# Optimization experiments

Measured on AMD Instinct MI355X. Metric: run time of the kernel, lower is better.

The kernel has to match this reference:

```python
import jax, jax.numpy as jnp
import numpy as np

CAPACITY_FACTOR = 1.0


def setup_inputs() -> dict:
    key = jax.random.key(0)
    k1, k2, k3, k4 = jax.random.split(key, 4)
    B, T, D, E, F = 4, 2048, 2048, 8, 8192
    hidden_states = jax.random.normal(k1, (B, T, D), dtype=jnp.float32)
    w_gate = jax.random.normal(k2, (D, E), dtype=jnp.float32) * 0.02
    w1 = jax.random.normal(k3, (E, D, F), dtype=jnp.float32) * 0.02
    w2 = jax.random.normal(k4, (E, F, D), dtype=jnp.float32) * 0.02
    return {"hidden_states": hidden_states, "w_gate": w_gate, "w1": w1, "w2": w2}


def _top1_gate(x, w_gate):
    # x: [S, D]; deepspeed top1gating (no noise, no rts, drop_tokens=True)
    S, E = x.shape[0], w_gate.shape[1]
    capacity = int(CAPACITY_FACTOR * S / E)
    logits = x @ w_gate                      # [S, E]
    gates = jax.nn.softmax(logits, axis=-1)  # [S, E]
    idx1 = jnp.argmax(gates, axis=-1)        # [S]
    mask1 = jax.nn.one_hot(idx1, E, dtype=gates.dtype)          # [S, E]
    locations1 = jnp.cumsum(mask1, axis=0) - mask1              # position within expert
    mask1 = mask1 * (locations1 < capacity)                     # drop over-capacity tokens
    locations1_s = jnp.sum(locations1 * mask1, axis=1).astype(jnp.int32)  # [S]
    gates_masked = gates * mask1                                # [S, E]
    loc_oh = jax.nn.one_hot(locations1_s, capacity, dtype=gates.dtype) * jnp.sum(mask1, axis=1, keepdims=True)
    combine_weights = jnp.einsum('se,sc->sec', gates_masked, loc_oh)      # [S, E, C]
    dispatch_mask = (combine_weights > 0).astype(gates.dtype)             # [S, E, C]
    return combine_weights, dispatch_mask


def reference(hidden_states, w_gate, w1, w2):
    B, T, D = hidden_states.shape
    x = hidden_states.reshape(-1, D)                     # [S, D]
    combine_weights, dispatch_mask = _top1_gate(x, w_gate)
    # dense dispatch: [S,E,C] x [S,D] -> [E,C,D]
    dispatched = jnp.einsum('sec,sm->ecm', dispatch_mask, x)
    # per-expert FFN (GELU MLP), batched over experts
    h = jax.nn.gelu(jnp.einsum('ecd,edf->ecf', dispatched, w1))
    expert_out = jnp.einsum('ecf,efd->ecd', h, w2)       # [E, C, D]
    # dense combine: [S,E,C] x [E,C,D] -> [S,D]
    combined = jnp.einsum('sec,ecm->sm', combine_weights, expert_out)
    return combined.reshape(B, T, D)
```

## Files before the change

### kernel.cpp

```cpp
#include <hip/hip_runtime.h>

using u16 = unsigned short;
typedef __attribute__((ext_vector_type(4))) float f32x4;
typedef __attribute__((ext_vector_type(8))) short bf16x8;
typedef unsigned short u16x8 __attribute__((ext_vector_type(8)));

static constexpr int S_TOK = 8192;
static constexpr int NE    = 8;
static constexpr int CAP   = 1024;
static constexpr int DDIM  = 2048;
static constexpr int FDIM  = 8192;

#define S_WAIT_ALL() asm volatile("s_waitcnt vmcnt(0) lgkmcnt(0)" ::: "memory")
#define S_BAR()                                  \
  do {                                           \
    __builtin_amdgcn_sched_barrier(0);           \
    __builtin_amdgcn_s_barrier();                \
    __builtin_amdgcn_sched_barrier(0);           \
  } while (0)

__device__ __forceinline__ u16 f2bf(float f) {
  union { float fv; unsigned uv; } v; v.fv = f;
  unsigned r = v.uv + 0x7fffu + ((v.uv >> 16) & 1u);
  return (u16)(r >> 16);
}

__device__ __forceinline__ unsigned cvt_pk_bf16(float lo, float hi) {
  unsigned r;
  asm("v_cvt_pk_bf16_f32 %0, %1, %2" : "=v"(r) : "v"(lo), "v"(hi));
  return r;
}

__device__ __forceinline__ float gelu_tanh(float x) {
  float u = 0.7978845608028654f * (x + 0.044715f * x * x * x);
  float t = 1.0f - 2.0f / (__expf(2.0f * u) + 1.0f);
  return 0.5f * x * (1.0f + t);
}

__device__ __forceinline__ void gl_lds16(const void* g, void* l) {
  __builtin_amdgcn_global_load_lds(
      (const __attribute__((address_space(1))) unsigned int*)g,
      (__attribute__((address_space(3))) unsigned int*)l, 16, 0, 0);
}

__global__ __launch_bounds__(256) void fill_zero_kernel(float4* __restrict__ p, int n4) {
  int i = blockIdx.x * 256 + threadIdx.x;
  int stride = gridDim.x * 256;
  float4 z = {0.f, 0.f, 0.f, 0.f};
  for (; i < n4; i += stride) p[i] = z;
}

__global__ __launch_bounds__(256) void gating_kernel(
    const float* __restrict__ x, const float* __restrict__ wg,
    int* __restrict__ tok_expert, float* __restrict__ tok_gate) {
  int s = blockIdx.x * 4 + (threadIdx.x >> 6);
  int lane = threadIdx.x & 63;
  const float4* xv = (const float4*)(x + (size_t)s * DDIM + lane * 32);
  float acc[8];
#pragma unroll
  for (int e = 0; e < 8; ++e) acc[e] = 0.f;
#pragma unroll
  for (int j = 0; j < 8; ++j) {
    float4 xx = xv[j];
#pragma unroll
    for (int c = 0; c < 4; ++c) {
      int i = lane * 32 + j * 4 + c;
      const float4* wrow = (const float4*)(wg + (size_t)i * 8);
      float4 w0 = wrow[0], w1 = wrow[1];
      float xe = (c == 0) ? xx.x : (c == 1) ? xx.y : (c == 2) ? xx.z : xx.w;
      acc[0] += xe * w0.x; acc[1] += xe * w0.y; acc[2] += xe * w0.z; acc[3] += xe * w0.w;
      acc[4] += xe * w1.x; acc[5] += xe * w1.y; acc[6] += xe * w1.z; acc[7] += xe * w1.w;
    }
  }
#pragma unroll
  for (int off = 32; off > 0; off >>= 1)
#pragma unroll
    for (int e = 0; e < 8; ++e) acc[e] += __shfl_xor(acc[e], off, 64);
  if (lane == 0) {
    float m = acc[0]; int ai = 0;
#pragma unroll
    for (int e = 1; e < 8; ++e) if (acc[e] > m) { m = acc[e]; ai = e; }
    float sum = 0.f;
#pragma unroll
    for (int e = 0; e < 8; ++e) sum += expf(acc[e] - m);
    tok_expert[s] = ai;
    tok_gate[s] = 1.0f / sum;
  }
}

__global__ __launch_bounds__(1024) void scan_kernel(
    const int* __restrict__ tok_expert, const float* __restrict__ tok_gate,
    int* __restrict__ tok_of_slot, float* __restrict__ gate_of_slot) {
  __shared__ int cnt[1024][8];
  int t = threadIdx.x;
  int e8[8];
  int local[8];
#pragma unroll
  for (int e = 0; e < 8; ++e) local[e] = 0;
#pragma unroll
  for (int j = 0; j < 8; ++j) {
    int e = tok_expert[t * 8 + j];
    e8[j] = e;
    local[e]++;
  }
#pragma unroll
  for (int e = 0; e < 8; ++e) cnt[t][e] = local[e];
  __syncthreads();
  for (int off = 1; off < 1024; off <<= 1) {
    int v[8];
    bool has = (t >= off);
    if (has) {
#pragma unroll
      for (int e = 0; e < 8; ++e) v[e] = cnt[t - off][e];
    }
    __syncthreads();
    if (has) {
#pragma unroll
      for (int e = 0; e < 8; ++e) cnt[t][e] += v[e];
    }
    __syncthreads();
  }
  int base[8];
#pragma unroll
  for (int e = 0; e < 8; ++e) base[e] = (t == 0) ? 0 : cnt[t - 1][e];
#pragma unroll
  for (int j = 0; j < 8; ++j) {
    int s = t * 8 + j;
    int e = e8[j];
    int p = base[e]++;
    if (p < CAP) {
      tok_of_slot[e * CAP + p] = s;
      gate_of_slot[e * CAP + p] = tok_gate[s];
    }
  }
#pragma unroll
  for (int e = 0; e < 8; ++e) {
    int total = cnt[1023][e];
    if (t >= total) {
      tok_of_slot[e * CAP + t] = -1;
      gate_of_slot[e * CAP + t] = 0.f;
    }
  }
}

__global__ __launch_bounds__(256) void scatter_kernel(
    const int* __restrict__ tok_of_slot, const float* __restrict__ x,
    u16* __restrict__ Xd) {
  int slot = blockIdx.x;
  int s = tok_of_slot[slot];
  int t = threadIdx.x;
  u16x8 v;
  if (s >= 0) {
    const float4* xr = (const float4*)(x + (size_t)s * DDIM + t * 8);
    float4 a = xr[0], b = xr[1];
    v[0] = f2bf(a.x); v[1] = f2bf(a.y); v[2] = f2bf(a.z); v[3] = f2bf(a.w);
    v[4] = f2bf(b.x); v[5] = f2bf(b.y); v[6] = f2bf(b.z); v[7] = f2bf(b.w);
  } else {
#pragma unroll
    for (int j = 0; j < 8; ++j) v[j] = 0;
  }
  *(u16x8*)(Xd + (size_t)slot * DDIM + t * 8) = v;
}

template <int KDIM, int NDIM, int EPI, int NEXP>
__global__ __launch_bounds__(512, 2) void moe_gemm(
    const u16* __restrict__ A, const float* __restrict__ Bf,
    u16* __restrict__ Hout, float* __restrict__ Fout,
    const int* __restrict__ tok_of_slot, const float* __restrict__ gate_of_slot,
    int e_base) {
  constexpr int MDIM = 1024;
  constexpr int BM = 256, BN = 256, BK = 64;
  constexpr int MT = MDIM / BM;
  constexpr int NK = KDIM / BK;
  constexpr int ASZ = BM * BK;
  constexpr int BSZ = BN * BK;
  constexpr int BUFSZ = ASZ + BSZ;
  __shared__ u16 lds[2 * BUFSZ];

  const int t = threadIdx.x;
  const int lane = t & 63, wave = t >> 6;
  const int wr = wave >> 2, wc = wave & 3;

  int id = blockIdx.x;
  int ez = id & (NEXP - 1);
  int w = id / NEXP;
  int mt = w & (MT - 1);
  int nt = w / MT;
  int m0 = mt * BM, n0 = nt * BN;
  int e = e_base + ez;

  const u16* Ae = A + (size_t)ez * MDIM * KDIM;
  const float* Be = Bf + (size_t)ez * (size_t)KDIM * NDIM;

  const u16* aSrc[4];
  int ldsOffA[4];
#pragma unroll
  for (int p = 0; p < 4; ++p) {
    int c = t + p * 512;
    int row = c >> 3;
    int fr = (row ^ (row >> 2)) & 7;
    int j = (c & 7) ^ fr;
    aSrc[p] = Ae + (size_t)(m0 + row) * KDIM + j * 8;
    ldsOffA[p] = c * 8;
  }

  const int bq = (t & 63) * 4;
  const int boct = t >> 6;
  const float* bP = Be + (size_t)(boct * 8) * NDIM + n0 + bq;
  int bWOff[4];
#pragma unroll
  for (int c = 0; c < 4; ++c) {
    int row = bq + c;
    int fr = (row ^ (row >> 2)) & 7;
    bWOff[c] = ASZ + row * 64 + (boct ^ fr) * 8;
  }

  const int r = lane & 15, h = lane >> 4;
  const int Kk = h ^ (r & 7) ^ (r >> 2);
  const int pE = Kk * 8;
  const int pO = (Kk ^ 4) * 8;
  const int aBase = (wr * 128 + r) * 64;
  const int bBase = ASZ + (wc * 64 + r) * 64;

  f32x4 acc[8][4];
#pragma unroll
  for (int m = 0; m < 8; ++m)
#pragma unroll
    for (int n = 0; n < 4; ++n) acc[m][n] = f32x4{0.f, 0.f, 0.f, 0.f};

  f32x4 bv4[8];

#pragma unroll
  for (int j = 0; j < 8; ++j) bv4[j] = *(const f32x4*)(bP + (size_t)j * NDIM);
#pragma unroll
  for (int p = 0; p < 4; ++p) gl_lds16(aSrc[p], &lds[ldsOffA[p]]);
#pragma unroll
  for (int c = 0; c < 4; ++c) {
    union { u16x8 v; unsigned w[4]; } o;
#pragma unroll
    for (int j = 0; j < 4; ++j) o.w[j] = cvt_pk_bf16(bv4[2 * j][c], bv4[2 * j + 1][c]);
    *(u16x8*)(&lds[bWOff[c]]) = o.v;
  }
  S_WAIT_ALL();
  S_BAR();

  for (int kt = 0; kt < NK; ++kt) {
    const u16* sb = &lds[(kt & 1) * BUFSZ];
    u16* nb = &lds[((kt + 1) & 1) * BUFSZ];
    const bool pre = (kt + 1 < NK);
    if (pre) {
      const int ko = (kt + 1) * BK;
#pragma unroll
      for (int p = 0; p < 4; ++p) gl_lds16(aSrc[p] + ko, nb + ldsOffA[p]);
#pragma unroll
      for (int j = 0; j < 8; ++j)
        bv4[j] = *(const f32x4*)(bP + (size_t)(ko + j) * NDIM);
    }

#pragma unroll
    for (int kk = 0; kk < 2; ++kk) {
      bf16x8 af[8], bv[4];
#pragma unroll
      for (int m = 0; m < 8; ++m)
        af[m] = *(const bf16x8*)(sb + aBase + m * 1024 + (((kk ^ m) & 1) ? pO : pE));
#pragma unroll
      for (int n = 0; n < 4; ++n)
        bv[n] = *(const bf16x8*)(sb + bBase + n * 1024 + (((kk ^ n) & 1) ? pO : pE));
      __builtin_amdgcn_s_setprio(1);
#pragma unroll
      for (int m = 0; m < 8; ++m)
#pragma unroll
        for (int n = 0; n < 4; ++n)
          acc[m][n] = __builtin_amdgcn_mfma_f32_16x16x32_bf16(af[m], bv[n], acc[m][n], 0, 0, 0);
      __builtin_amdgcn_s_setprio(0);
    }

    if (pre) {
#pragma unroll
      for (int c = 0; c < 4; ++c) {
        union { u16x8 v; unsigned w[4]; } o;
#pragma unroll
        for (int j = 0; j < 4; ++j) o.w[j] = cvt_pk_bf16(bv4[2 * j][c], bv4[2 * j + 1][c]);
        *(u16x8*)(nb + bWOff[c]) = o.v;
      }
    }
    S_WAIT_ALL();
    S_BAR();
  }

  if (EPI == 0) {
    u16* Hrow = Hout + (size_t)ez * MDIM * NDIM;
#pragma unroll
    for (int m = 0; m < 8; ++m) {
#pragma unroll
      for (int rr = 0; rr < 4; ++rr) {
        int row = m0 + wr * 128 + m * 16 + h * 4 + rr;
#pragma unroll
        for (int n = 0; n < 4; ++n) {
          int col = n0 + wc * 64 + n * 16 + r;
          Hrow[(size_t)row * NDIM + col] = f2bf(gelu_tanh(acc[m][n][rr]));
        }
      }
    }
  } else {
#pragma unroll
    for (int m = 0; m < 8; ++m) {
#pragma unroll
      for (int rr = 0; rr < 4; ++rr) {
        int slot_in_e = m0 + wr * 128 + m * 16 + h * 4 + rr;
        int gslot = e * CAP + slot_in_e;
        int s = tok_of_slot[gslot];
        if (s >= 0) {
          float g = gate_of_slot[gslot];
#pragma unroll
          for (int n = 0; n < 4; ++n) {
            int col = n0 + wc * 64 + n * 16 + r;
            Fout[(size_t)s * NDIM + col] = g * acc[m][n][rr];
          }
        }
      }
    }
  }
}

extern "C" void kernel_launch(void* const* d_in, const int* in_sizes, int n_in,
                              void* d_out, int out_size, void* d_ws, size_t ws_size,
                              hipStream_t stream) {
  (void)in_sizes; (void)n_in;
  const float* x  = (const float*)d_in[0];
  const float* wg = (const float*)d_in[1];
  const float* w1 = (const float*)d_in[2];
  const float* w2 = (const float*)d_in[3];
  float* out = (float*)d_out;

  char* ws = (char*)d_ws;
  size_t off = 0;
  auto alloc = [&](size_t b) {
    off = (off + 255) & ~(size_t)255;
    char* p = ws + off;
    off += b;
    return p;
  };
  int*   tok_expert   = (int*)alloc((size_t)S_TOK * 4);
  float* tok_gate     = (float*)alloc((size_t)S_TOK * 4);
  int*   tok_of_slot  = (int*)alloc((size_t)NE * CAP * 4);
  float* gate_of_slot = (float*)alloc((size_t)NE * CAP * 4);
  u16*   Xd           = (u16*)alloc((size_t)NE * CAP * DDIM * 2);
  size_t off_common = off;

  const size_t H_big = (size_t)NE * CAP * FDIM * 2;
  const size_t H_sm  = (size_t)CAP * FDIM * 2;
  bool big = ws_size >= off_common + H_big + 1024;

  fill_zero_kernel<<<2048, 256, 0, stream>>>((float4*)out, out_size / 4);
  gating_kernel<<<S_TOK / 4, 256, 0, stream>>>(x, wg, tok_expert, tok_gate);
  scan_kernel<<<1, 1024, 0, stream>>>(tok_expert, tok_gate, tok_of_slot, gate_of_slot);
  scatter_kernel<<<NE * CAP, 256, 0, stream>>>(tok_of_slot, x, Xd);

  if (big) {
    u16* H = (u16*)alloc(H_big);
    moe_gemm<DDIM, FDIM, 0, NE><<<dim3(NE * 4 * (FDIM / 256)), 512, 0, stream>>>(
        Xd, w1, H, nullptr, tok_of_slot, gate_of_slot, 0);
    moe_gemm<FDIM, DDIM, 1, NE><<<dim3(NE * 4 * (DDIM / 256)), 512, 0, stream>>>(
        H, w2, nullptr, out, tok_of_slot, gate_of_slot, 0);
  } else {
    u16* H = (u16*)alloc(H_sm);
    for (int e = 0; e < NE; ++e) {
      moe_gemm<DDIM, FDIM, 0, 1><<<dim3(4 * (FDIM / 256)), 512, 0, stream>>>(
          Xd + (size_t)e * CAP * DDIM, w1 + (size_t)e * DDIM * FDIM, H, nullptr,
          tok_of_slot, gate_of_slot, e);
      moe_gemm<FDIM, DDIM, 1, 1><<<dim3(4 * (DDIM / 256)), 512, 0, stream>>>(
          H, w2 + (size_t)e * FDIM * DDIM, nullptr, out,
          tok_of_slot, gate_of_slot, e);
    }
  }
}
```

Measured before the change: 716.3 us.

## Prefetch fp32 B tiles two K-steps ahead with partial vmcnt waits

Restructures the GEMM main loop so the fp32 weight tile loads run two K-iterations ahead in alternating register sets (bvE/bvO). The loop is unrolled by two with fixed LDS buffers, and the full waitcnt is replaced by partial vmcnt waits. The aim is to hide global-load latency of the weight stream behind MFMA work instead of stalling at every barrier. In exchange it uses 32 more VGPRs per thread under launch_bounds(512,2), which risks spilling. It also issues redundant clamped loads near the end of K and relies on exact outstanding-load counts for correctness.

Result: slower. 1.145 ms (+59.9%).

```diff
diff --git a/kernel.cpp b/kernel.cpp
--- a/kernel.cpp
+++ b/kernel.cpp
@@ -11,7 +11,9 @@
 static constexpr int DDIM  = 2048;
 static constexpr int FDIM  = 8192;
 
-#define S_WAIT_ALL() asm volatile("s_waitcnt vmcnt(0) lgkmcnt(0)" ::: "memory")
+#define S_VM12() asm volatile("s_waitcnt vmcnt(12)" ::: "memory")
+#define S_VM8()  asm volatile("s_waitcnt vmcnt(8)" ::: "memory")
+#define LGKM0()  asm volatile("s_waitcnt lgkmcnt(0)" ::: "memory")
 #define S_BAR()                                  \
   do {                                           \
     __builtin_amdgcn_sched_barrier(0);           \
@@ -160,6 +162,42 @@
     for (int j = 0; j < 8; ++j) v[j] = 0;
   }
   *(u16x8*)(Xd + (size_t)slot * DDIM + t * 8) = v;
+}
+
+__device__ __forceinline__ void loadB8(const float* bP, int ko, int nd, f32x4 (&bv)[8]) {
+#pragma unroll
+  for (int j = 0; j < 8; ++j) bv[j] = *(const f32x4*)(bP + (size_t)(ko + j) * nd);
+}
+
+__device__ __forceinline__ void cvt_writeB(u16* nb, const int (&bWOff)[4], const f32x4 (&bv)[8]) {
+#pragma unroll
+  for (int c = 0; c < 4; ++c) {
+    union { u16x8 v; unsigned w[4]; } o;
+#pragma unroll
+    for (int j = 0; j < 4; ++j) o.w[j] = cvt_pk_bf16(bv[2 * j][c], bv[2 * j + 1][c]);
+    *(u16x8*)(nb + bWOff[c]) = o.v;
+  }
+}
+
+__device__ __forceinline__ void mfma_body(const u16* sb, int aBase, int bBase,
+                                          int pE, int pO, f32x4 (&acc)[8][4]) {
+#pragma unroll
+  for (int kk = 0; kk < 2; ++kk) {
+    bf16x8 af[8], bv[4];
+#pragma unroll
+    for (int m = 0; m < 8; ++m)
+      af[m] = *(const bf16x8*)(sb + aBase + m * 1024 + (((kk ^ m) & 1) ? pO : pE));
+#pragma unroll
+    for (int n = 0; n < 4; ++n)
+      bv[n] = *(const bf16x8*)(sb + bBase + n * 1024 + (((kk ^ n) & 1) ? pO : pE));
+    __builtin_amdgcn_s_setprio(1);
+#pragma unroll
+    for (int m = 0; m < 8; ++m)
+#pragma unroll
+      for (int n = 0; n < 4; ++n)
+        acc[m][n] = __builtin_amdgcn_mfma_f32_16x16x32_bf16(af[m], bv[n], acc[m][n], 0, 0, 0);
+    __builtin_amdgcn_s_setprio(0);
+  }
 }
 
 template <int KDIM, int NDIM, int EPI, int NEXP>
@@ -228,64 +266,54 @@
 #pragma unroll
     for (int n = 0; n < 4; ++n) acc[m][n] = f32x4{0.f, 0.f, 0.f, 0.f};
 
-  f32x4 bv4[8];
-
-#pragma unroll
-  for (int j = 0; j < 8; ++j) bv4[j] = *(const f32x4*)(bP + (size_t)j * NDIM);
+  f32x4 bvE[8], bvO[8];
+
+  loadB8(bP, 0, NDIM, bvE);
 #pragma unroll
   for (int p = 0; p < 4; ++p) gl_lds16(aSrc[p], &lds[ldsOffA[p]]);
-#pragma unroll
-  for (int c = 0; c < 4; ++c) {
-    union { u16x8 v; unsigned w[4]; } o;
-#pragma unroll
-    for (int j = 0; j < 4; ++j) o.w[j] = cvt_pk_bf16(bv4[2 * j][c], bv4[2 * j + 1][c]);
-    *(u16x8*)(&lds[bWOff[c]]) = o.v;
-  }
-  S_WAIT_ALL();
+  loadB8(bP, BK, NDIM, bvO);
+  S_VM12();
+  cvt_writeB(&lds[0], bWOff, bvE);
+  S_VM8();
+  LGKM0();
   S_BAR();
 
-  for (int kt = 0; kt < NK; ++kt) {
-    const u16* sb = &lds[(kt & 1) * BUFSZ];
-    u16* nb = &lds[((kt + 1) & 1) * BUFSZ];
-    const bool pre = (kt + 1 < NK);
-    if (pre) {
-      const int ko = (kt + 1) * BK;
-#pragma unroll
-      for (int p = 0; p < 4; ++p) gl_lds16(aSrc[p] + ko, nb + ldsOffA[p]);
-#pragma unroll
-      for (int j = 0; j < 8; ++j)
-        bv4[j] = *(const f32x4*)(bP + (size_t)(ko + j) * NDIM);
-    }
-
-#pragma unroll
-    for (int kk = 0; kk < 2; ++kk) {
-      bf16x8 af[8], bv[4];
-#pragma unroll
-      for (int m = 0; m < 8; ++m)
-        af[m] = *(const bf16x8*)(sb + aBase + m * 1024 + (((kk ^ m) & 1) ? pO : pE));
-#pragma unroll
-      for (int n = 0; n < 4; ++n)
-        bv[n] = *(const bf16x8*)(sb + bBase + n * 1024 + (((kk ^ n) & 1) ? pO : pE));
-      __builtin_amdgcn_s_setprio(1);
-#pragma unroll
-      for (int m = 0; m < 8; ++m)
-#pragma unroll
-        for (int n = 0; n < 4; ++n)
-          acc[m][n] = __builtin_amdgcn_mfma_f32_16x16x32_bf16(af[m], bv[n], acc[m][n], 0, 0, 0);
-      __builtin_amdgcn_s_setprio(0);
-    }
-
-    if (pre) {
-#pragma unroll
-      for (int c = 0; c < 4; ++c) {
-        union { u16x8 v; unsigned w[4]; } o;
-#pragma unroll
-        for (int j = 0; j < 4; ++j) o.w[j] = cvt_pk_bf16(bv4[2 * j][c], bv4[2 * j + 1][c]);
-        *(u16x8*)(nb + bWOff[c]) = o.v;
-      }
-    }
-    S_WAIT_ALL();
-    S_BAR();
+  const int koLast = KDIM - BK;
+  for (int kt = 0; kt < NK; kt += 2) {
+    {
+      const u16* sb = &lds[0];
+      u16* nb = &lds[BUFSZ];
+      int ko1 = (kt + 1) * BK; if (ko1 > koLast) ko1 = koLast;
+      int ko2 = (kt + 2) * BK; if (ko2 > koLast) ko2 = koLast;
+#pragma unroll
+      for (int p = 0; p < 4; ++p) gl_lds16(aSrc[p] + ko1, nb + ldsOffA[p]);
+      loadB8(bP, ko2, NDIM, bvE);
+
+      mfma_body(sb, aBase, bBase, pE, pO, acc);
+
+      S_VM12();
+      cvt_writeB(nb, bWOff, bvO);
+      S_VM8();
+      LGKM0();
+      S_BAR();
+    }
+    {
+      const u16* sb = &lds[BUFSZ];
+      u16* nb = &lds[0];
+      int ko1 = (kt + 2) * BK; if (ko1 > koLast) ko1 = koLast;
+      int ko2 = (kt + 3) * BK; if (ko2 > koLast) ko2 = koLast;
+#pragma unroll
+      for (int p = 0; p < 4; ++p) gl_lds16(aSrc[p] + ko1, nb + ldsOffA[p]);
+      loadB8(bP, ko2, NDIM, bvO);
+
+      mfma_body(sb, aBase, bBase, pE, pO, acc);
+
+      S_VM12();
+      cvt_writeB(nb, bWOff, bvE);
+      S_VM8();
+      LGKM0();
+      S_BAR();
+    }
   }
 
   if (EPI == 0) {
```
